# Performance work log

Hardware: AMD Instinct MI355X
Metric: run time of the kernel (lower is better)

The kernel has to match this reference:

```python
import jax, jax.numpy as jnp
import numpy as np

FT = 0.2  # clip floor (init arg ft)

def _norm_mat(m):
    # matrix / (count of nonzeros along last dim + 1e-30)
    deg = jnp.sum(m != 0, axis=-1, keepdims=True).astype(m.dtype)
    return m / (deg + 1e-30)

def _l2n(x):
    return x / (jnp.linalg.norm(x, axis=-1, keepdims=True) + 1e-30)

def setup_inputs():
    B, L, D, H, O = 2, 2048, 64, 64, 128
    N = 2 * L
    ks = jax.random.split(jax.random.key(0), 30)
    u = lambda i, s: jax.random.uniform(ks[i], s, jnp.float32)
    g = lambda i, s: jax.random.normal(ks[i], s, jnp.float32) * 0.05
    inp = {}
    inp['word_outputs_0'] = g(0, (B, L, D))
    inp['word_outputs_1'] = g(1, (B, L, D))
    inp['node_hidden'] = g(2, (B, D))
    inp['op_embedding'] = g(3, (B, O, D))
    inp['word_exist_sequence'] = (u(4, (B, N)) < 0.8).astype(jnp.float32)
    inp['word_exist_matrix'] = (u(5, (B, N, N)) < 0.8).astype(jnp.float32)
    inp['word_operator'] = (u(6, (B, N, O)) < 0.02).astype(jnp.float32)
    inp['word_word'] = (u(7, (B, N, N)) < 0.01).astype(jnp.float32)
    inp['depend_0'] = (u(8, (B, L, L)) < 0.05).astype(jnp.float32)
    inp['depend_1'] = (u(9, (B, L, L)) < 0.05).astype(jnp.float32)
    inp['goal_word'] = u(10, (B, N))
    names = [('Wg', (D, H)), ('bg', (H,)), ('Wwk', (D, H)), ('bwk', (H,)),
             ('Wws', (D, H)), ('bws', (H,)), ('Wo', (D, D)), ('bo', (D,)),
             ('Wupd', (3 * H, D)), ('bupd', (D,)), ('Wf', (3 * H + D, D)), ('bf', (D,)),
             ('Wf2', (2 * D, D)), ('bf2', (D,)), ('Wout', (D, D)), ('bout', (D,))]
    for i, (nm, s) in enumerate(names):
        inp[nm] = g(11 + i, s)
    return inp

def _forward(w0, w1, nh, opE, wes, wem, wop, ww, d0, d1, gw,
             Wg, bg, Wwk, bwk, Wws, bws, Wo, bo, Wupd, bupd, Wf, bf, Wf2, bf2, Wout, bout):
    all_w = jnp.concatenate([w0, w1], axis=1)                      # [B,N,D]
    goal_trans = (nh @ Wg + bg)[:, None, :]                        # [B,1,H] (broadcast = expand)
    word_g = _l2n(goal_trans * gw[..., None])                      # [B,N,H]
    word_w_k = _l2n(jnp.matmul(_norm_mat(ww * wem), all_w @ Wwk + bwk))
    ws0 = jnp.matmul(_norm_mat(d0), w0 @ Wws + bws)
    ws1 = jnp.matmul(_norm_mat(d1), w1 @ Wws + bws)
    word_w_s = _l2n(jnp.concatenate([ws0, ws1], axis=1))           # [B,N,H]
    neigh = jnp.concatenate([word_g, word_w_k, word_w_s], axis=-1)  # [B,N,3H]
    forget = jax.nn.sigmoid(jnp.concatenate([all_w, word_g, word_w_k, word_w_s], axis=-1) @ Wf + bf)
    word_updated = jnp.maximum(forget, FT) * all_w + (1.0 - forget) * jax.nn.relu(neigh @ Wupd + bupd)
    adj_op = _norm_mat(jnp.swapaxes(wes[..., None] * wop, 1, 2))   # [B,O,N]
    word_op = jnp.matmul(adj_op, word_updated @ Wo + bo)           # [B,O,D]
    forget2 = jax.nn.sigmoid(jnp.concatenate([opE, word_op], axis=-1) @ Wf2 + bf2)
    op_out = jnp.maximum(forget2, FT) * opE + (1.0 - forget2) * jax.nn.relu(word_op @ Wout + bout)
    # original returns (split(word_updated), op_embedding); concat along node axis here
    return jnp.concatenate([word_updated, op_out], axis=1)         # [B,N+O,D]

def reference(word_outputs_0, word_outputs_1, node_hidden, op_embedding,
              word_exist_sequence, word_exist_matrix, word_operator, word_word,
              depend_0, depend_1, goal_word,
              Wg, bg, Wwk, bwk, Wws, bws, Wo, bo, Wupd, bupd, Wf, bf, Wf2, bf2, Wout, bout):
    return _forward(word_outputs_0, word_outputs_1, node_hidden, op_embedding,
                    word_exist_sequence, word_exist_matrix, word_operator, word_word,
                    depend_0, depend_1, goal_word,
                    Wg, bg, Wwk, bwk, Wws, bws, Wo, bo, Wupd, bupd, Wf, bf, Wf2, bf2, Wout, bout)
```

## Files before the change

### kernel.cpp

```cpp
#include <hip/hip_runtime.h>
#include <cstdint>

typedef unsigned short u16;
typedef unsigned long long u64;

__device__ __forceinline__ u16 f2b(float f){
  union { float f; uint32_t i; } v; v.f = f;
  uint32_t r = v.i + 0x7FFFu + ((v.i >> 16) & 1u);
  return (u16)(r >> 16);
}
__device__ __forceinline__ float b2f(u16 u){
  union { uint32_t i; float f; } v; v.i = ((uint32_t)u) << 16; return v.f;
}
__device__ __forceinline__ float sigmoidf(float x){ return 1.0f / (1.0f + __expf(-x)); }

__global__ void k_pre(const float* __restrict__ nh, const float* __restrict__ Wg,
                      const float* __restrict__ bg, float* __restrict__ ghat){
  int b = threadIdx.x >> 6, h = threadIdx.x & 63;
  float g = bg[h];
  for (int d = 0; d < 64; ++d) g += nh[b*64 + d] * Wg[d*64 + h];
  float ss = g * g;
  #pragma unroll
  for (int o = 32; o > 0; o >>= 1) ss += __shfl_xor(ss, o, 64);
  ghat[b*64 + h] = g / (sqrtf(ss) + 1e-30f);
}

__global__ __launch_bounds__(256) void k_xform(
    const float* __restrict__ w0, const float* __restrict__ w1,
    const float* __restrict__ Wwk, const float* __restrict__ bwk,
    const float* __restrict__ Wws, const float* __restrict__ bws,
    float* __restrict__ Xk, float* __restrict__ Xs){
  __shared__ float sWk[4096], sWs[4096];
  int tid = threadIdx.x;
  for (int i = tid; i < 1024; i += 256){
    ((float4*)sWk)[i] = ((const float4*)Wwk)[i];
    ((float4*)sWs)[i] = ((const float4*)Wws)[i];
  }
  __syncthreads();
  int lane = tid & 63, wave = tid >> 6;
  float bk = bwk[lane], bs = bws[lane];
  float aw[4];
  #pragma unroll
  for (int t = 0; t < 4; ++t){
    int row = blockIdx.x*4 + wave + t*2048;
    int b = row >> 12, n = row & 4095;
    aw[t] = (n < 2048) ? w0[((size_t)(b*2048 + n))*64 + lane]
                       : w1[((size_t)(b*2048 + n - 2048))*64 + lane];
  }
  #pragma unroll
  for (int t = 0; t < 4; ++t){
    int row = blockIdx.x*4 + wave + t*2048;
    float xk = bk, xs = bs;
    #pragma unroll 8
    for (int d = 0; d < 64; ++d){
      float a = __shfl(aw[t], d, 64);
      xk += a * sWk[d*64 + lane];
      xs += a * sWs[d*64 + lane];
    }
    Xk[(size_t)row*64 + lane] = xk;
    Xs[(size_t)row*64 + lane] = xs;
  }
}

template<bool TWO, int JS>
__global__ __launch_bounds__(256) void k_bits(
    const float* __restrict__ A, const float* __restrict__ B, u64* __restrict__ bits){
  int lane = threadIdx.x & 63, wave = threadIdx.x >> 6;
  int row = blockIdx.x*4 + wave;
  const float* a = A + (size_t)row * (JS*256) + lane*4;
  const float* bb = TWO ? (B + (size_t)row * (JS*256) + lane*4) : nullptr;
  u64 myword = 0;
  #pragma unroll 4
  for (int j = 0; j < JS; ++j){
    float4 va = *(const float4*)(a + j*256);
    float4 vb;
    if (TWO) vb = *(const float4*)(bb + j*256);
    #pragma unroll
    for (int s = 0; s < 4; ++s){
      float x = (s==0)?va.x:(s==1)?va.y:(s==2)?va.z:va.w;
      bool nz = (x != 0.f);
      if (TWO){
        float y = (s==0)?vb.x:(s==1)?vb.y:(s==2)?vb.z:vb.w;
        nz = nz && (y != 0.f);
      }
      u64 m = __ballot(nz);
      if (lane == j*4 + s) myword = m;
    }
  }
  if (lane < JS*4) bits[(size_t)row*(JS*4) + lane] = myword;
}

__global__ __launch_bounds__(256) void k_bitsop(
    const float* __restrict__ wes, const float* __restrict__ wop, u64* __restrict__ bitOp){
  int lane = threadIdx.x & 63, wave = threadIdx.x >> 6;
  int wg = blockIdx.x*4 + wave;
  for (int it = 0; it < 16; ++it){
    int ng = wg*16 + it;
    float2 v = ((const float2*)(wop + (size_t)ng*128))[lane];
    float e = wes[ng];
    u64 m0 = __ballot(e != 0.f && v.x != 0.f);
    u64 m1 = __ballot(e != 0.f && v.y != 0.f);
    if (lane == 0) bitOp[(size_t)ng*2]     = m0;
    if (lane == 1) bitOp[(size_t)ng*2 + 1] = m1;
  }
}

__global__ __launch_bounds__(256) void k_gath(
    const u64* __restrict__ bits, const float* __restrict__ X,
    u16* __restrict__ outp, int rowsPB, int WPR, int xoff){
  __shared__ int q[4][256];
  int lane = threadIdx.x & 63, wave = threadIdx.x >> 6;
  int rowIdx = blockIdx.x*4 + wave;
  int b = rowIdx / rowsPB, r = rowIdx - b*rowsPB;
  u64 word = (lane < WPR) ? bits[(size_t)rowIdx*WPR + lane] : 0ULL;
  int c = __popcll(word);
  int pre = c;
  #pragma unroll
  for (int off = 1; off < 64; off <<= 1){
    int t = __shfl_up(pre, off, 64);
    if (lane >= off) pre += t;
  }
  int total = __shfl(pre, 63, 64);
  int base = pre - c;
  int colhi = (lane >> 2) * 256 + (lane & 3);
  u64 m = word;
  while (m){
    int p = __builtin_ctzll(m); m &= m - 1;
    q[wave][base++] = colhi + p*4;
  }
  __syncthreads();
  const float* Xb = X + ((size_t)b*4096 + xoff)*64 + lane;
  float acc = 0.f;
  int i = 0;
  for (; i + 8 <= total; i += 8){
    int4 c0 = *(const int4*)&q[wave][i];
    int4 c1 = *(const int4*)&q[wave][i + 4];
    float v0 = Xb[(size_t)c0.x*64], v1 = Xb[(size_t)c0.y*64];
    float v2 = Xb[(size_t)c0.z*64], v3 = Xb[(size_t)c0.w*64];
    float v4 = Xb[(size_t)c1.x*64], v5 = Xb[(size_t)c1.y*64];
    float v6 = Xb[(size_t)c1.z*64], v7 = Xb[(size_t)c1.w*64];
    acc += ((v0 + v1) + (v2 + v3)) + ((v4 + v5) + (v6 + v7));
  }
  for (; i < total; ++i) acc += Xb[(size_t)q[wave][i]*64];
  float ss = acc * acc;
  #pragma unroll
  for (int o = 32; o > 0; o >>= 1) ss += __shfl_xor(ss, o, 64);
  outp[((size_t)b*4096 + xoff + r)*64 + lane] = f2b(acc / (sqrtf(ss) + 1e-30f));
}

__global__ __launch_bounds__(256, 2) void k_update(
    const float* __restrict__ w0, const float* __restrict__ w1,
    const float* __restrict__ gw, const float* __restrict__ ghat,
    const u16* __restrict__ wwkn, const u16* __restrict__ wwsn,
    const float* __restrict__ Wf, const float* __restrict__ bf,
    const float* __restrict__ Wupd, const float* __restrict__ bupd,
    float* __restrict__ out, float* __restrict__ WU){
  __shared__ uint32_t pWf[128*64];
  __shared__ uint32_t pWu[96*64];
  __shared__ float xsh[4][256];
  int tid = threadIdx.x;
  for (int i = tid; i < 8192; i += 256){
    int k2 = i >> 6, ln = i & 63;
    pWf[i] = (uint32_t)f2b(Wf[(2*k2)*64 + ln]) | ((uint32_t)f2b(Wf[(2*k2+1)*64 + ln]) << 16);
  }
  for (int i = tid; i < 6144; i += 256){
    int k2 = i >> 6, ln = i & 63;
    pWu[i] = (uint32_t)f2b(Wupd[(2*k2)*64 + ln]) | ((uint32_t)f2b(Wupd[(2*k2+1)*64 + ln]) << 16);
  }
  __syncthreads();
  int lane = tid & 63, wave = tid >> 6;
  float bff = bf[lane], bup = bupd[lane];
  float aw[4], wgv[4], wk[4], wsv[4];
  #pragma unroll
  for (int t = 0; t < 4; ++t){
    int row = blockIdx.x*4 + wave + t*2048;
    int b = row >> 12, n = row & 4095;
    aw[t] = (n < 2048) ? w0[((size_t)(b*2048 + n))*64 + lane]
                       : w1[((size_t)(b*2048 + n - 2048))*64 + lane];
    float gvv = gw[b*4096 + n];
    wgv[t] = (gvv != 0.f) ? ghat[b*64 + lane] : 0.f;
    wk[t]  = b2f(wwkn[(size_t)row*64 + lane]);
    wsv[t] = b2f(wwsn[(size_t)row*64 + lane]);
  }
  #pragma unroll
  for (int t = 0; t < 4; ++t){
    int row = blockIdx.x*4 + wave + t*2048;
    int b = row >> 12, n = row & 4095;
    xsh[wave][lane] = aw[t]; xsh[wave][64 + lane] = wgv[t];
    xsh[wave][128 + lane] = wk[t]; xsh[wave][192 + lane] = wsv[t];
    float f = bff, u = bup;
    #pragma unroll 8
    for (int k2 = 0; k2 < 32; ++k2){
      float2 xv = *(const float2*)&xsh[wave][2*k2];
      uint32_t wf = pWf[k2*64 + lane];
      f += xv.x * b2f((u16)wf) + xv.y * b2f((u16)(wf >> 16));
    }
    #pragma unroll 8
    for (int k2 = 32; k2 < 128; ++k2){
      float2 xv = *(const float2*)&xsh[wave][2*k2];
      uint32_t wf = pWf[k2*64 + lane];
      uint32_t wu = pWu[(k2 - 32)*64 + lane];
      f += xv.x * b2f((u16)wf) + xv.y * b2f((u16)(wf >> 16));
      u += xv.x * b2f((u16)wu) + xv.y * b2f((u16)(wu >> 16));
    }
    f = sigmoidf(f);
    u = fmaxf(u, 0.f);
    float wu = fmaxf(f, 0.2f) * aw[t] + (1.f - f) * u;
    out[((size_t)b*4224 + n)*64 + lane] = wu;
    WU[(size_t)row*64 + lane] = wu;
  }
}

__global__ __launch_bounds__(256) void k_wuo(
    const float* __restrict__ WU, const float* __restrict__ Wo,
    const float* __restrict__ bo, float* __restrict__ WUo){
  __shared__ float sWo[4096];
  int tid = threadIdx.x;
  for (int i = tid; i < 1024; i += 256) ((float4*)sWo)[i] = ((const float4*)Wo)[i];
  __syncthreads();
  int lane = tid & 63, wave = tid >> 6;
  float boo = bo[lane];
  float wu[4];
  #pragma unroll
  for (int t = 0; t < 4; ++t){
    int row = blockIdx.x*4 + wave + t*2048;
    wu[t] = WU[(size_t)row*64 + lane];
  }
  #pragma unroll
  for (int t = 0; t < 4; ++t){
    int row = blockIdx.x*4 + wave + t*2048;
    float o = boo;
    #pragma unroll 8
    for (int d = 0; d < 64; ++d) o += __shfl(wu[t], d, 64) * sWo[d*64 + lane];
    WUo[(size_t)row*64 + lane] = o;
  }
}

__global__ __launch_bounds__(256) void k_opagg(
    const u64* __restrict__ bitOp, const float* __restrict__ WUo,
    float* __restrict__ wordop){
  __shared__ int q[4][256];
  int lane = threadIdx.x & 63, wave = threadIdx.x >> 6;
  int rowIdx = blockIdx.x*4 + wave;
  int b = rowIdx >> 7, o = rowIdx & 127;
  int wrd = o & 1, bit = o >> 1;
  const u64* bp = bitOp + (size_t)b*4096*2 + wrd;
  u64 lt = (1ULL << lane) - 1ULL;
  int cnt = 0;
  #pragma unroll 4
  for (int it = 0; it < 64; ++it){
    int n = it*64 + lane;
    u64 v = bp[(size_t)n*2];
    bool nz = (v >> bit) & 1ULL;
    u64 m = __ballot(nz);
    if (nz) q[wave][cnt + (int)__popcll(m & lt)] = n;
    cnt += (int)__popcll(m);
  }
  __syncthreads();
  const float* Xb = WUo + (size_t)b*4096*64 + lane;
  float acc = 0.f;
  int i = 0;
  for (; i + 8 <= cnt; i += 8){
    int4 c0 = *(const int4*)&q[wave][i];
    int4 c1 = *(const int4*)&q[wave][i + 4];
    float v0 = Xb[(size_t)c0.x*64], v1 = Xb[(size_t)c0.y*64];
    float v2 = Xb[(size_t)c0.z*64], v3 = Xb[(size_t)c0.w*64];
    float v4 = Xb[(size_t)c1.x*64], v5 = Xb[(size_t)c1.y*64];
    float v6 = Xb[(size_t)c1.z*64], v7 = Xb[(size_t)c1.w*64];
    acc += ((v0 + v1) + (v2 + v3)) + ((v4 + v5) + (v6 + v7));
  }
  for (; i < cnt; ++i) acc += Xb[(size_t)q[wave][i]*64];
  wordop[(size_t)rowIdx*64 + lane] = acc / ((float)cnt + 1e-30f);
}

__global__ __launch_bounds__(256) void k_opout(
    const float* __restrict__ opE, const float* __restrict__ wordop,
    const float* __restrict__ Wf2, const float* __restrict__ bf2,
    const float* __restrict__ Wout, const float* __restrict__ bout,
    float* __restrict__ out){
  __shared__ float sW2[8192];
  __shared__ float sWo[4096];
  __shared__ float xsh[4][128];
  int tid = threadIdx.x;
  for (int i = tid; i < 2048; i += 256) ((float4*)sW2)[i] = ((const float4*)Wf2)[i];
  for (int i = tid; i < 1024; i += 256) ((float4*)sWo)[i] = ((const float4*)Wout)[i];
  __syncthreads();
  int lane = tid & 63, wave = tid >> 6;
  int row = blockIdx.x*4 + wave;
  int b = row >> 7, o = row & 127;
  float e  = opE[(size_t)row*64 + lane];
  float wo = wordop[(size_t)row*64 + lane];
  xsh[wave][lane] = e; xsh[wave][64 + lane] = wo;
  float f = bf2[lane], u = bout[lane];
  #pragma unroll 8
  for (int k = 0; k < 128; ++k) f += xsh[wave][k] * sW2[k*64 + lane];
  #pragma unroll 8
  for (int d = 0; d < 64; ++d)  u += xsh[wave][64 + d] * sWo[d*64 + lane];
  f = sigmoidf(f);
  u = fmaxf(u, 0.f);
  float res = fmaxf(f, 0.2f) * e + (1.f - f) * u;
  out[((size_t)b*4224 + 4096 + o)*64 + lane] = res;
}

extern "C" void kernel_launch(void* const* d_in, const int* in_sizes, int n_in,
                              void* d_out, int out_size, void* d_ws, size_t ws_size,
                              hipStream_t stream){
  const float* w0   = (const float*)d_in[0];
  const float* w1   = (const float*)d_in[1];
  const float* nh   = (const float*)d_in[2];
  const float* opE  = (const float*)d_in[3];
  const float* wes  = (const float*)d_in[4];
  const float* wem  = (const float*)d_in[5];
  const float* wop  = (const float*)d_in[6];
  const float* ww   = (const float*)d_in[7];
  const float* d0   = (const float*)d_in[8];
  const float* d1   = (const float*)d_in[9];
  const float* gw   = (const float*)d_in[10];
  const float* Wg   = (const float*)d_in[11];
  const float* bg   = (const float*)d_in[12];
  const float* Wwk  = (const float*)d_in[13];
  const float* bwk  = (const float*)d_in[14];
  const float* Wws  = (const float*)d_in[15];
  const float* bws  = (const float*)d_in[16];
  const float* Wo   = (const float*)d_in[17];
  const float* bo   = (const float*)d_in[18];
  const float* Wupd = (const float*)d_in[19];
  const float* bupd = (const float*)d_in[20];
  const float* Wf   = (const float*)d_in[21];
  const float* bf   = (const float*)d_in[22];
  const float* Wf2  = (const float*)d_in[23];
  const float* bf2  = (const float*)d_in[24];
  const float* Wout = (const float*)d_in[25];
  const float* bout = (const float*)d_in[26];

  float* ws   = (float*)d_ws;
  float* ghat = ws;
  float* Xk   = ws + 128;
  float* Xs   = ws + 524416;
  float* wopm = ws + 1048704;
  u16*  wwkn  = (u16*)(ws + 1065088);
  u16*  wwsn  = (u16*)(ws + 1327232);
  u64*  bitBig= (u64*)(ws + 1589376);
  u64*  bitD0 = (u64*)(ws + 2637952);
  u64*  bitD1 = (u64*)(ws + 2900096);
  u64*  bitOp = (u64*)(ws + 3162240);
  float* WU   = Xk;
  float* WUo  = Xs;
  float* out  = (float*)d_out;

  k_pre<<<1, 128, 0, stream>>>(nh, Wg, bg, ghat);
  k_xform<<<512, 256, 0, stream>>>(w0, w1, Wwk, bwk, Wws, bws, Xk, Xs);
  k_bits<true , 16><<<2048, 256, 0, stream>>>(ww, wem, bitBig);
  k_bits<false, 8 ><<<1024, 256, 0, stream>>>(d0, nullptr, bitD0);
  k_bits<false, 8 ><<<1024, 256, 0, stream>>>(d1, nullptr, bitD1);
  k_bitsop<<<128, 256, 0, stream>>>(wes, wop, bitOp);
  k_gath<<<2048, 256, 0, stream>>>(bitBig, Xk, wwkn, 4096, 64, 0);
  k_gath<<<1024, 256, 0, stream>>>(bitD0, Xs, wwsn, 2048, 32, 0);
  k_gath<<<1024, 256, 0, stream>>>(bitD1, Xs, wwsn, 2048, 32, 2048);
  k_update<<<512, 256, 0, stream>>>(w0, w1, gw, ghat, wwkn, wwsn, Wf, bf, Wupd, bupd, out, WU);
  k_wuo<<<512, 256, 0, stream>>>(WU, Wo, bo, WUo);
  k_opagg<<<64, 256, 0, stream>>>(bitOp, WUo, wopm);
  k_opout<<<64, 256, 0, stream>>>(opE, wopm, Wf2, bf2, Wout, bout, out);
}
```

Measured before the change: 507.4 us.

## Merge bit-mask and gather kernels, fuse Wo projection, split op aggregation

Combines the three mask-packing launches into one kernel in which each wave handles 1024 columns, and the three gather launches into one kernel. The Wo projection moves into k_update using bf16-packed weights in LDS, which removes the WU round trip and the separate k_wuo launch. k_opagg now uses four waves per operator row, each scanning a quarter of the nodes, then reduces their partial sums in shared memory, giving more parallelism than one wave per row. k_bitsop now runs one 64-thread block per node. The changes cut launch count and raise occupancy in the small kernels, at the cost of more LDS in k_update and bf16 rounding of Wo.

```diff
diff --git a/kernel.cpp b/kernel.cpp
--- a/kernel.cpp
+++ b/kernel.cpp
@@ -62,57 +62,76 @@
   }
 }
 
-template<bool TWO, int JS>
-__global__ __launch_bounds__(256) void k_bits(
-    const float* __restrict__ A, const float* __restrict__ B, u64* __restrict__ bits){
-  int lane = threadIdx.x & 63, wave = threadIdx.x >> 6;
-  int row = blockIdx.x*4 + wave;
-  const float* a = A + (size_t)row * (JS*256) + lane*4;
-  const float* bb = TWO ? (B + (size_t)row * (JS*256) + lane*4) : nullptr;
-  u64 myword = 0;
-  #pragma unroll 4
-  for (int j = 0; j < JS; ++j){
-    float4 va = *(const float4*)(a + j*256);
-    float4 vb;
-    if (TWO) vb = *(const float4*)(bb + j*256);
-    #pragma unroll
-    for (int s = 0; s < 4; ++s){
-      float x = (s==0)?va.x:(s==1)?va.y:(s==2)?va.z:va.w;
-      bool nz = (x != 0.f);
-      if (TWO){
-        float y = (s==0)?vb.x:(s==1)?vb.y:(s==2)?vb.z:vb.w;
-        nz = nz && (y != 0.f);
-      }
-      u64 m = __ballot(nz);
-      if (lane == j*4 + s) myword = m;
-    }
-  }
-  if (lane < JS*4) bits[(size_t)row*(JS*4) + lane] = myword;
-}
-
-__global__ __launch_bounds__(256) void k_bitsop(
+__global__ __launch_bounds__(256) void k_bits_all(
+    const float* __restrict__ ww, const float* __restrict__ wem,
+    const float* __restrict__ d0, const float* __restrict__ d1,
+    u64* __restrict__ bitBig, u64* __restrict__ bitD0, u64* __restrict__ bitD1){
+  int wid = blockIdx.x*4 + (threadIdx.x >> 6);
+  int lane = threadIdx.x & 63;
+  const float *A, *B; u64* dst;
+  if (wid < 32768){
+    A = ww + (size_t)wid*1024; B = wem + (size_t)wid*1024; dst = bitBig + (size_t)wid*16;
+  } else if (wid < 40960){
+    size_t c = wid - 32768; A = d0 + c*1024; B = A; dst = bitD0 + c*16;
+  } else {
+    size_t c = wid - 40960; A = d1 + c*1024; B = A; dst = bitD1 + c*16;
+  }
+  const float4* ap = (const float4*)A + lane;
+  const float4* bp = (const float4*)B + lane;
+  float4 a0 = ap[0], a1 = ap[64], a2 = ap[128], a3 = ap[192];
+  float4 b0 = bp[0], b1 = bp[64], b2 = bp[128], b3 = bp[192];
+  u64 myw = 0;
+#define B4(i, va, vb) { \
+  u64 m0 = __ballot((va.x != 0.f) && (vb.x != 0.f)); \
+  u64 m1 = __ballot((va.y != 0.f) && (vb.y != 0.f)); \
+  u64 m2 = __ballot((va.z != 0.f) && (vb.z != 0.f)); \
+  u64 m3 = __ballot((va.w != 0.f) && (vb.w != 0.f)); \
+  if (lane == (i)*4 + 0) myw = m0; \
+  if (lane == (i)*4 + 1) myw = m1; \
+  if (lane == (i)*4 + 2) myw = m2; \
+  if (lane == (i)*4 + 3) myw = m3; }
+  B4(0, a0, b0) B4(1, a1, b1) B4(2, a2, b2) B4(3, a3, b3)
+#undef B4
+  if (lane < 16) dst[lane] = myw;
+}
+
+__global__ __launch_bounds__(64) void k_bitsop(
     const float* __restrict__ wes, const float* __restrict__ wop, u64* __restrict__ bitOp){
-  int lane = threadIdx.x & 63, wave = threadIdx.x >> 6;
-  int wg = blockIdx.x*4 + wave;
-  for (int it = 0; it < 16; ++it){
-    int ng = wg*16 + it;
-    float2 v = ((const float2*)(wop + (size_t)ng*128))[lane];
-    float e = wes[ng];
-    u64 m0 = __ballot(e != 0.f && v.x != 0.f);
-    u64 m1 = __ballot(e != 0.f && v.y != 0.f);
-    if (lane == 0) bitOp[(size_t)ng*2]     = m0;
-    if (lane == 1) bitOp[(size_t)ng*2 + 1] = m1;
-  }
-}
-
-__global__ __launch_bounds__(256) void k_gath(
-    const u64* __restrict__ bits, const float* __restrict__ X,
-    u16* __restrict__ outp, int rowsPB, int WPR, int xoff){
+  int lane = threadIdx.x;
+  int ng = blockIdx.x;
+  float2 v = ((const float2*)(wop + (size_t)ng*128))[lane];
+  float e = wes[ng];
+  u64 m0 = __ballot((e != 0.f) && (v.x != 0.f));
+  u64 m1 = __ballot((e != 0.f) && (v.y != 0.f));
+  if (lane == 0) bitOp[(size_t)ng*2]     = m0;
+  if (lane == 1) bitOp[(size_t)ng*2 + 1] = m1;
+}
+
+__global__ __launch_bounds__(256) void k_gath_all(
+    const u64* __restrict__ bitBig, const u64* __restrict__ bitD0, const u64* __restrict__ bitD1,
+    const float* __restrict__ Xk, const float* __restrict__ Xs,
+    u16* __restrict__ wwkn, u16* __restrict__ wwsn){
   __shared__ int q[4][256];
   int lane = threadIdx.x & 63, wave = threadIdx.x >> 6;
-  int rowIdx = blockIdx.x*4 + wave;
-  int b = rowIdx / rowsPB, r = rowIdx - b*rowsPB;
-  u64 word = (lane < WPR) ? bits[(size_t)rowIdx*WPR + lane] : 0ULL;
+  int wid = blockIdx.x*4 + wave;
+  const u64* bits; const float* Xb; u16* op; int WPR;
+  if (wid < 8192){
+    WPR = 64; bits = bitBig + (size_t)wid*64;
+    int b = wid >> 12;
+    Xb = Xk + (size_t)b*4096*64 + lane;
+    op = wwkn + (size_t)wid*64;
+  } else if (wid < 12288){
+    int lr = wid - 8192; WPR = 32; bits = bitD0 + (size_t)lr*32;
+    int b = lr >> 11, r = lr & 2047;
+    Xb = Xs + (size_t)b*4096*64 + lane;
+    op = wwsn + ((size_t)b*4096 + r)*64;
+  } else {
+    int lr = wid - 12288; WPR = 32; bits = bitD1 + (size_t)lr*32;
+    int b = lr >> 11, r = lr & 2047;
+    Xb = Xs + ((size_t)b*4096 + 2048)*64 + lane;
+    op = wwsn + ((size_t)b*4096 + 2048 + r)*64;
+  }
+  u64 word = (lane < WPR) ? bits[lane] : 0ULL;
   int c = __popcll(word);
   int pre = c;
   #pragma unroll
@@ -129,7 +148,6 @@
     q[wave][base++] = colhi + p*4;
   }
   __syncthreads();
-  const float* Xb = X + ((size_t)b*4096 + xoff)*64 + lane;
   float acc = 0.f;
   int i = 0;
   for (; i + 8 <= total; i += 8){
@@ -145,7 +163,7 @@
   float ss = acc * acc;
   #pragma unroll
   for (int o = 32; o > 0; o >>= 1) ss += __shfl_xor(ss, o, 64);
-  outp[((size_t)b*4096 + xoff + r)*64 + lane] = f2b(acc / (sqrtf(ss) + 1e-30f));
+  op[lane] = f2b(acc / (sqrtf(ss) + 1e-30f));
 }
 
 __global__ __launch_bounds__(256, 2) void k_update(
@@ -154,9 +172,11 @@
     const u16* __restrict__ wwkn, const u16* __restrict__ wwsn,
     const float* __restrict__ Wf, const float* __restrict__ bf,
     const float* __restrict__ Wupd, const float* __restrict__ bupd,
-    float* __restrict__ out, float* __restrict__ WU){
-  __shared__ uint32_t pWf[128*64];
-  __shared__ uint32_t pWu[96*64];
+    const float* __restrict__ Wo, const float* __restrict__ bo,
+    float* __restrict__ out, float* __restrict__ WUo){
+  __shared__ uint32_t pWf[8192];
+  __shared__ uint32_t pWu[6144];
+  __shared__ uint32_t pWo[2048];
   __shared__ float xsh[4][256];
   int tid = threadIdx.x;
   for (int i = tid; i < 8192; i += 256){
@@ -167,9 +187,13 @@
     int k2 = i >> 6, ln = i & 63;
     pWu[i] = (uint32_t)f2b(Wupd[(2*k2)*64 + ln]) | ((uint32_t)f2b(Wupd[(2*k2+1)*64 + ln]) << 16);
   }
+  for (int i = tid; i < 2048; i += 256){
+    int k2 = i >> 6, ln = i & 63;
+    pWo[i] = (uint32_t)f2b(Wo[(2*k2)*64 + ln]) | ((uint32_t)f2b(Wo[(2*k2+1)*64 + ln]) << 16);
+  }
   __syncthreads();
   int lane = tid & 63, wave = tid >> 6;
-  float bff = bf[lane], bup = bupd[lane];
+  float bff = bf[lane], bup = bupd[lane], boo = bo[lane];
   float aw[4], wgv[4], wk[4], wsv[4];
   #pragma unroll
   for (int t = 0; t < 4; ++t){
@@ -207,31 +231,12 @@
     u = fmaxf(u, 0.f);
     float wu = fmaxf(f, 0.2f) * aw[t] + (1.f - f) * u;
     out[((size_t)b*4224 + n)*64 + lane] = wu;
-    WU[(size_t)row*64 + lane] = wu;
-  }
-}
-
-__global__ __launch_bounds__(256) void k_wuo(
-    const float* __restrict__ WU, const float* __restrict__ Wo,
-    const float* __restrict__ bo, float* __restrict__ WUo){
-  __shared__ float sWo[4096];
-  int tid = threadIdx.x;
-  for (int i = tid; i < 1024; i += 256) ((float4*)sWo)[i] = ((const float4*)Wo)[i];
-  __syncthreads();
-  int lane = tid & 63, wave = tid >> 6;
-  float boo = bo[lane];
-  float wu[4];
-  #pragma unroll
-  for (int t = 0; t < 4; ++t){
-    int row = blockIdx.x*4 + wave + t*2048;
-    wu[t] = WU[(size_t)row*64 + lane];
-  }
-  #pragma unroll
-  for (int t = 0; t < 4; ++t){
-    int row = blockIdx.x*4 + wave + t*2048;
     float o = boo;
     #pragma unroll 8
-    for (int d = 0; d < 64; ++d) o += __shfl(wu[t], d, 64) * sWo[d*64 + lane];
+    for (int k2 = 0; k2 < 32; ++k2){
+      uint32_t wo2 = pWo[k2*64 + lane];
+      o += __shfl(wu, 2*k2, 64) * b2f((u16)wo2) + __shfl(wu, 2*k2 + 1, 64) * b2f((u16)(wo2 >> 16));
+    }
     WUo[(size_t)row*64 + lane] = o;
   }
 }
@@ -239,24 +244,26 @@
 __global__ __launch_bounds__(256) void k_opagg(
     const u64* __restrict__ bitOp, const float* __restrict__ WUo,
     float* __restrict__ wordop){
-  __shared__ int q[4][256];
-  int lane = threadIdx.x & 63, wave = threadIdx.x >> 6;
-  int rowIdx = blockIdx.x*4 + wave;
+  __shared__ int q[4][96];
+  __shared__ float sacc[4][64];
+  __shared__ int scnt[4];
+  int tid = threadIdx.x, lane = tid & 63, wave = tid >> 6;
+  int rowIdx = blockIdx.x;
   int b = rowIdx >> 7, o = rowIdx & 127;
   int wrd = o & 1, bit = o >> 1;
-  const u64* bp = bitOp + (size_t)b*4096*2 + wrd;
+  const u64* bp = bitOp + (size_t)b*8192 + (size_t)wave*2048 + wrd;
   u64 lt = (1ULL << lane) - 1ULL;
+  u64 vv[16];
+  #pragma unroll
+  for (int it = 0; it < 16; ++it) vv[it] = bp[(size_t)(it*64 + lane)*2];
   int cnt = 0;
-  #pragma unroll 4
-  for (int it = 0; it < 64; ++it){
-    int n = it*64 + lane;
-    u64 v = bp[(size_t)n*2];
-    bool nz = (v >> bit) & 1ULL;
+  #pragma unroll
+  for (int it = 0; it < 16; ++it){
+    bool nz = (vv[it] >> bit) & 1ULL;
     u64 m = __ballot(nz);
-    if (nz) q[wave][cnt + (int)__popcll(m & lt)] = n;
+    if (nz) q[wave][cnt + (int)__popcll(m & lt)] = wave*1024 + it*64 + lane;
     cnt += (int)__popcll(m);
   }
-  __syncthreads();
   const float* Xb = WUo + (size_t)b*4096*64 + lane;
   float acc = 0.f;
   int i = 0;
@@ -270,7 +277,14 @@
     acc += ((v0 + v1) + (v2 + v3)) + ((v4 + v5) + (v6 + v7));
   }
   for (; i < cnt; ++i) acc += Xb[(size_t)q[wave][i]*64];
-  wordop[(size_t)rowIdx*64 + lane] = acc / ((float)cnt + 1e-30f);
+  sacc[wave][lane] = acc;
+  if (lane == 0) scnt[wave] = cnt;
+  __syncthreads();
+  if (wave == 0){
+    float t = sacc[0][lane] + sacc[1][lane] + sacc[2][lane] + sacc[3][lane];
+    float deg = (float)(scnt[0] + scnt[1] + scnt[2] + scnt[3]);
+    wordop[(size_t)rowIdx*64 + lane] = t / (deg + 1e-30f);
+  }
 }
 
 __global__ __launch_bounds__(256) void k_opout(
@@ -338,27 +352,21 @@
   float* Xk   = ws + 128;
   float* Xs   = ws + 524416;
   float* wopm = ws + 1048704;
-  u16*  wwkn  = (u16*)(ws + 1065088);
-  u16*  wwsn  = (u16*)(ws + 1327232);
-  u64*  bitBig= (u64*)(ws + 1589376);
-  u64*  bitD0 = (u64*)(ws + 2637952);
-  u64*  bitD1 = (u64*)(ws + 2900096);
-  u64*  bitOp = (u64*)(ws + 3162240);
-  float* WU   = Xk;
+  u64*  bitBig= (u64*)(ws + 1065088);
+  u64*  bitD0 = (u64*)(ws + 2113664);
+  u64*  bitD1 = (u64*)(ws + 2375808);
+  u64*  bitOp = (u64*)(ws + 2637952);
+  u16*  wwkn  = (u16*)(ws + 2670720);
+  u16*  wwsn  = (u16*)(ws + 2932864);
   float* WUo  = Xs;
   float* out  = (float*)d_out;
 
   k_pre<<<1, 128, 0, stream>>>(nh, Wg, bg, ghat);
   k_xform<<<512, 256, 0, stream>>>(w0, w1, Wwk, bwk, Wws, bws, Xk, Xs);
-  k_bits<true , 16><<<2048, 256, 0, stream>>>(ww, wem, bitBig);
-  k_bits<false, 8 ><<<1024, 256, 0, stream>>>(d0, nullptr, bitD0);
-  k_bits<false, 8 ><<<1024, 256, 0, stream>>>(d1, nullptr, bitD1);
-  k_bitsop<<<128, 256, 0, stream>>>(wes, wop, bitOp);
-  k_gath<<<2048, 256, 0, stream>>>(bitBig, Xk, wwkn, 4096, 64, 0);
-  k_gath<<<1024, 256, 0, stream>>>(bitD0, Xs, wwsn, 2048, 32, 0);
-  k_gath<<<1024, 256, 0, stream>>>(bitD1, Xs, wwsn, 2048, 32, 2048);
-  k_update<<<512, 256, 0, stream>>>(w0, w1, gw, ghat, wwkn, wwsn, Wf, bf, Wupd, bupd, out, WU);
-  k_wuo<<<512, 256, 0, stream>>>(WU, Wo, bo, WUo);
-  k_opagg<<<64, 256, 0, stream>>>(bitOp, WUo, wopm);
+  k_bits_all<<<12288, 256, 0, stream>>>(ww, wem, d0, d1, bitBig, bitD0, bitD1);
+  k_bitsop<<<8192, 64, 0, stream>>>(wes, wop, bitOp);
+  k_gath_all<<<4096, 256, 0, stream>>>(bitBig, bitD0, bitD1, Xk, Xs, wwkn, wwsn);
+  k_update<<<512, 256, 0, stream>>>(w0, w1, gw, ghat, wwkn, wwsn, Wf, bf, Wupd, bupd, Wo, bo, out, WUo);
+  k_opagg<<<256, 256, 0, stream>>>(bitOp, WUo, wopm);
   k_opout<<<64, 256, 0, stream>>>(opE, wopm, Wf2, bf2, Wout, bout, out);
 }
```

Measured after the change: 456.7 us. 1.11x faster.
